# Optimization experiments

Hardware: AMD Instinct MI355X
Metric: run time of the kernel (lower is better)

## Reference

```python
import jax, jax.numpy as jnp
import numpy as np

EPS = 1e-3

def _block_orthogonal(num_rows, num_cols, seed=0):
    # Faithful to orthogonal_matrix(): stack of QR-orthogonalized square blocks.
    rng = np.random.default_rng(seed)
    blocks = []
    n_full = num_rows // num_cols
    for _ in range(n_full):
        q, _ = np.linalg.qr(rng.standard_normal((num_cols, num_cols)).astype(np.float32))
        blocks.append(q.T)
    remain = num_rows - n_full * num_cols
    if remain > 0:
        q, _ = np.linalg.qr(rng.standard_normal((num_cols, num_cols)).astype(np.float32))
        blocks.append(q.T[:remain])
    return jnp.asarray(np.concatenate(blocks, axis=0), dtype=jnp.float32)


def setup_inputs() -> dict:
    key = jax.random.key(0)
    k1, k2, k3 = jax.random.split(key, 3)
    B, H, L, D = 4, 16, 4096, 64
    num_rows = int(D * np.log(D))  # 266
    return {
        "q": jax.random.normal(k1, (B, H, L, D), dtype=jnp.float32),
        "k": jax.random.normal(k2, (B, H, L, D), dtype=jnp.float32),
        "v": jax.random.normal(k3, (B, H, L, D), dtype=jnp.float32),
        "proj_mat": _block_orthogonal(num_rows, D),  # [266, 64]
    }


def _feature_map(x, proj_t):
    # x: [b,h,l,d], proj_t: [d,m] -> [b,h,l,m]; kernel = relu, +epsilon
    return jax.nn.relu(jnp.einsum('bhld,dm->bhlm', x, proj_t)) + EPS


def reference(q, k, v, proj_mat):
    proj_t = proj_mat.T                     # [d, m]
    qp = _feature_map(q, proj_t)            # [b,h,l,m]
    kp = _feature_map(k, proj_t)            # [b,h,l,m]
    k_sum = jnp.sum(kp, axis=-2)            # [b,h,m]
    d_inv = 1.0 / jnp.einsum('bhlm,bhm->bhl', qp, k_sum)   # [b,h,l]
    kv = jnp.einsum('bhlm,bhld->bhmd', kp, v)              # [b,h,m,d]
    qkv = jnp.einsum('bhlm,bhmd->bhld', qp, kv)            # [b,h,l,d]
    return qkv * d_inv[..., None]
```

## Files before the change

### kernel.cpp

```cpp
#include <hip/hip_runtime.h>

typedef __bf16 bf16;
typedef bf16 bf16x2 __attribute__((ext_vector_type(2)));
typedef bf16 bf16x4 __attribute__((ext_vector_type(4)));
typedef bf16 bf16x8 __attribute__((ext_vector_type(8)));
typedef float f32x4 __attribute__((ext_vector_type(4)));
typedef float f32x16 __attribute__((ext_vector_type(16)));
typedef unsigned int u32;
typedef u32 u32x4 __attribute__((ext_vector_type(4)));
typedef float4 f4;

constexpr int BHN = 64;
constexpr int LN  = 4096;
constexpr int DN  = 64;
constexpr int MN  = 266;
constexpr int MP  = 320;
constexpr int STR = 72;
constexpr int KVS = 328;
constexpr int TL  = 128;
constexpr int NLQ = 4;
constexpr int NTQ = LN / (NLQ * TL);
#define EPSF 1e-3f

#define MFMA32(A, B, C) __builtin_amdgcn_mfma_f32_32x32x16_bf16(A, B, C, 0, 0, 0)

__device__ __forceinline__ u32 cvt_pk_bf16(float lo, float hi) {
  u32 r;
  asm("v_cvt_pk_bf16_f32 %0, %1, %2" : "=v"(r) : "v"(lo), "v"(hi));
  return r;
}

#define T12_TRANSFORM(f, kb0, kb1)                                   \
  {                                                                  \
    u32 w0 = cvt_pk_bf16(f[0], f[1]);                                \
    u32 w1 = cvt_pk_bf16(f[2], f[3]);                                \
    u32 w2 = cvt_pk_bf16(f[4], f[5]);                                \
    u32 w3 = cvt_pk_bf16(f[6], f[7]);                                \
    u32 w4 = cvt_pk_bf16(f[8], f[9]);                                \
    u32 w5 = cvt_pk_bf16(f[10], f[11]);                              \
    u32 w6 = cvt_pk_bf16(f[12], f[13]);                              \
    u32 w7 = cvt_pk_bf16(f[14], f[15]);                              \
    asm("v_permlane32_swap_b32 %0, %1" : "+v"(w0), "+v"(w2));        \
    asm("v_permlane32_swap_b32 %0, %1" : "+v"(w1), "+v"(w3));        \
    asm("v_permlane32_swap_b32 %0, %1" : "+v"(w4), "+v"(w6));        \
    asm("v_permlane32_swap_b32 %0, %1" : "+v"(w5), "+v"(w7));        \
    u32x4 a0_ = {w0, w1, w2, w3};                                    \
    u32x4 a1_ = {w4, w5, w6, w7};                                    \
    kb0 = __builtin_bit_cast(bf16x8, a0_);                           \
    kb1 = __builtin_bit_cast(bf16x8, a1_);                           \
  }

__global__ __launch_bounds__(640, 2) void perf_kv_fused(
    const float* __restrict__ kg, const float* __restrict__ vg,
    const float* __restrict__ proj, float* __restrict__ kv_part,
    float* __restrict__ ksum_part)
{
  __shared__ __align__(16) bf16 k_lds[TL * STR];
  __shared__ __align__(16) bf16 vt_lds[64 * 128];

  const int t    = threadIdx.x;
  const int wid  = t >> 6;
  const int lane = t & 63;
  const int ln31 = lane & 31;
  const int hi   = lane >> 5;
  const int mc   = wid % 5;
  const int h    = wid / 5;
  const int lq   = blockIdx.x & 3;
  const int bh   = blockIdx.x >> 2;
  const int m0   = mc * 64;

  bf16x8 pb[4];
  {
    const int m = m0 + h * 32 + ln31;
#pragma unroll
    for (int ks = 0; ks < 4; ++ks) {
      bf16x8 w = {};
      if (m < MN) {
        const float* p = proj + m * 64 + ks * 16 + hi * 8;
        f4 a = *(const f4*)p;
        f4 b = *(const f4*)(p + 4);
        w = (bf16x8){(bf16)a.x, (bf16)a.y, (bf16)a.z, (bf16)a.w,
                     (bf16)b.x, (bf16)b.y, (bf16)b.z, (bf16)b.w};
      }
      pb[ks] = w;
    }
  }

  f32x16 acc0 = (f32x16){};
  f32x16 acc1 = (f32x16){};
  float ksum_acc = 0.f;

  const f4* kg4 = (const f4*)kg + ((size_t)bh * LN) * 16;
  const f4* vg4 = (const f4*)vg + ((size_t)bh * LN) * 16;

  f4 kreg[4], vra[2], vrb[2];

  auto LOAD = [&](int tile) {
    const int l0 = (lq * NTQ + tile) * TL;
    if (t < 512) {
#pragma unroll
      for (int i2 = 0; i2 < 4; ++i2) {
        int idx = t + i2 * 512;
        kreg[i2] = kg4[(l0 + (idx >> 4)) * 16 + (idx & 15)];
      }
#pragma unroll
      for (int i2 = 0; i2 < 2; ++i2) {
        int u = t + i2 * 512;
        int lb2 = u >> 4, d4 = u & 15;
        vra[i2] = vg4[(l0 + lb2 * 2) * 16 + d4];
        vrb[i2] = vg4[(l0 + lb2 * 2 + 1) * 16 + d4];
      }
    }
  };
  auto VTW = [&](int r, int c) -> bf16* {
    return &vt_lds[r * 128 + (c ^ ((r & 15) << 3))];
  };
  auto WRITE = [&]() {
    if (t < 512) {
#pragma unroll
      for (int i2 = 0; i2 < 4; ++i2) {
        int idx = t + i2 * 512;
        int row = idx >> 4, d4 = idx & 15;
        f4 val = kreg[i2];
        bf16x4 w = {(bf16)val.x, (bf16)val.y, (bf16)val.z, (bf16)val.w};
        *(bf16x4*)&k_lds[row * STR + d4 * 4] = w;
      }
#pragma unroll
      for (int i2 = 0; i2 < 2; ++i2) {
        int u = t + i2 * 512;
        int lb2 = u >> 4, d4 = u & 15;
        f4 a = vra[i2], b = vrb[i2];
        bf16x2 w0 = {(bf16)a.x, (bf16)b.x};
        bf16x2 w1 = {(bf16)a.y, (bf16)b.y};
        bf16x2 w2 = {(bf16)a.z, (bf16)b.z};
        bf16x2 w3 = {(bf16)a.w, (bf16)b.w};
        *(bf16x2*)VTW(d4 * 4 + 0, lb2 * 2) = w0;
        *(bf16x2*)VTW(d4 * 4 + 1, lb2 * 2) = w1;
        *(bf16x2*)VTW(d4 * 4 + 2, lb2 * 2) = w2;
        *(bf16x2*)VTW(d4 * 4 + 3, lb2 * 2) = w3;
      }
    }
  };

  LOAD(0);
  for (int tile = 0; tile < NTQ; ++tile) {
    __syncthreads();
    WRITE();
    if (tile < NTQ - 1) LOAD(tile + 1);
    __syncthreads();

#pragma unroll
    for (int s4 = 0; s4 < 4; ++s4) {
      bf16x8 ka[4];
#pragma unroll
      for (int ks = 0; ks < 4; ++ks)
        ka[ks] = *(const bf16x8*)&k_lds[(s4 * 32 + ln31) * STR + ks * 16 + hi * 8];
      bf16x8 va00 = *(const bf16x8*)VTW(ln31, s4 * 32 + hi * 8);
      bf16x8 va01 = *(const bf16x8*)VTW(ln31, s4 * 32 + 16 + hi * 8);
      bf16x8 va10 = *(const bf16x8*)VTW(32 + ln31, s4 * 32 + hi * 8);
      bf16x8 va11 = *(const bf16x8*)VTW(32 + ln31, s4 * 32 + 16 + hi * 8);

      f32x16 f = (f32x16){};
#pragma unroll
      for (int ks = 0; ks < 4; ++ks) f = MFMA32(ka[ks], pb[ks], f);
#pragma unroll
      for (int i2 = 0; i2 < 16; ++i2) f[i2] = fmaxf(f[i2], 0.f) + EPSF;
      ksum_acc += f[0] + f[1] + f[2] + f[3] + f[4] + f[5] + f[6] + f[7]
                + f[8] + f[9] + f[10] + f[11] + f[12] + f[13] + f[14] + f[15];

      bf16x8 kb0, kb1;
      T12_TRANSFORM(f, kb0, kb1)
      acc0 = MFMA32(va00, kb0, acc0);
      acc0 = MFMA32(va01, kb1, acc0);
      acc1 = MFMA32(va10, kb0, acc1);
      acc1 = MFMA32(va11, kb1, acc1);
    }
  }

  {
    const int m = m0 + h * 32 + ln31;
    float* base = kv_part + ((size_t)lq * BHN + bh) * 64 * MP;
#pragma unroll
    for (int r = 0; r < 16; ++r) {
      const int d0 = (r & 3) + 8 * (r >> 2) + 4 * hi;
      base[(size_t)d0 * MP + m] = acc0[r];
      base[(size_t)(32 + d0) * MP + m] = acc1[r];
    }
    float rr = ksum_acc + __shfl_xor(ksum_acc, 32);
    if (hi == 0) ksum_part[((size_t)lq * BHN + bh) * MP + m] = rr;
  }
}

__global__ __launch_bounds__(256) void perf_reduce(
    const float* __restrict__ kv_part, const float* __restrict__ ksum_part,
    bf16* __restrict__ kv_b, float* __restrict__ ksum_ws)
{
  constexpr int KV4 = BHN * DN * MP / 4;
  constexpr int KS  = BHN * MP;
  constexpr size_t PS  = (size_t)BHN * DN * MP;
  constexpr size_t PSK = (size_t)BHN * MP;

  int idx = blockIdx.x * 256 + threadIdx.x;
  if (idx < KV4) {
    const f4* p = (const f4*)kv_part;
    f4 v0 = p[idx];
    f4 v1 = p[idx + PS / 4];
    f4 v2 = p[idx + 2 * (PS / 4)];
    f4 v3 = p[idx + 3 * (PS / 4)];
    f4 sv = {v0.x + v1.x + v2.x + v3.x, v0.y + v1.y + v2.y + v3.y,
             v0.z + v1.z + v2.z + v3.z, v0.w + v1.w + v2.w + v3.w};
    int m = (idx * 4) % MP;
    bf16x4 w;
    w[0] = (m + 0 < MN) ? (bf16)sv.x : (bf16)0.f;
    w[1] = (m + 1 < MN) ? (bf16)sv.y : (bf16)0.f;
    w[2] = (m + 2 < MN) ? (bf16)sv.z : (bf16)0.f;
    w[3] = (m + 3 < MN) ? (bf16)sv.w : (bf16)0.f;
    *(bf16x4*)&kv_b[idx * 4] = w;
  } else if (idx < KV4 + KS) {
    int p = idx - KV4;
    int m = p % MP;
    float v = ksum_part[p] + ksum_part[p + PSK] + ksum_part[p + 2 * PSK]
            + ksum_part[p + 3 * PSK];
    ksum_ws[p] = (m < MN) ? v : 0.f;
  }
}

__global__ __launch_bounds__(512, 2) void perf_out_mfma32(
    const float* __restrict__ qg, const float* __restrict__ proj,
    const bf16* __restrict__ kvb, const float* __restrict__ ksum_ws,
    float* __restrict__ outg)
{
  __shared__ __align__(16) bf16 pj_lds[MP * STR];
  __shared__ __align__(16) bf16 kv_lds[DN * KVS];
  __shared__ __align__(16) float ksum_lds[MP];
  __shared__ float dp_lds[8 * 64];

  const int t    = threadIdx.x;
  const int wid  = t >> 6;
  const int lane = t & 63;
  const int ln31 = lane & 31;
  const int hi   = lane >> 5;
  const int bh   = blockIdx.y;
  const int lbase = blockIdx.x * 1024;

  {
    const f4* projv = (const f4*)proj;
#pragma unroll
    for (int i = 0; i < 10; ++i) {
      int idx = t + i * 512;
      int r = idx >> 4, c4 = idx & 15;
      f4 v = {0.f, 0.f, 0.f, 0.f};
      if (r < MN) v = projv[r * 16 + c4];
      bf16x4 w = {(bf16)v.x, (bf16)v.y, (bf16)v.z, (bf16)v.w};
      *(bf16x4*)&pj_lds[r * STR + c4 * 4] = w;
    }
  }
  for (int idx = t; idx < DN * 40; idx += 512) {
    int r = idx / 40, cc = idx % 40;
    *(bf16x8*)&kv_lds[r * KVS + cc * 8] =
        *(const bf16x8*)&kvb[((size_t)bh * DN + r) * MP + cc * 8];
  }
  if (t < MP) ksum_lds[t] = ksum_ws[bh * MP + t];
  __syncthreads();

  for (int rnd = 0; rnd < 2; ++rnd) {
    const int lw = lbase + rnd * 512 + wid * 64;

    bf16x8 qb[2][4];
#pragma unroll
    for (int lt = 0; lt < 2; ++lt)
#pragma unroll
      for (int ks = 0; ks < 4; ++ks) {
        const float* qp_ = qg + ((size_t)bh * LN + lw + lt * 32 + ln31) * 64 + ks * 16 + hi * 8;
        f4 a = *(const f4*)qp_;
        f4 b = *(const f4*)(qp_ + 4);
        qb[lt][ks] = (bf16x8){(bf16)a.x, (bf16)a.y, (bf16)a.z, (bf16)a.w,
                              (bf16)b.x, (bf16)b.y, (bf16)b.z, (bf16)b.w};
      }

    f32x16 oc[2][2];
    oc[0][0] = (f32x16){}; oc[0][1] = (f32x16){};
    oc[1][0] = (f32x16){}; oc[1][1] = (f32x16){};
    float dp[2] = {0.f, 0.f};

    for (int mc = 0; mc < 5; ++mc) {
      f32x16 c2[2][2];
      c2[0][0] = (f32x16){}; c2[0][1] = (f32x16){};
      c2[1][0] = (f32x16){}; c2[1][1] = (f32x16){};
#pragma unroll
      for (int ks = 0; ks < 4; ++ks) {
        bf16x8 pa0 = *(const bf16x8*)&pj_lds[(mc * 64 + ln31) * STR + ks * 16 + hi * 8];
        bf16x8 pa1 = *(const bf16x8*)&pj_lds[(mc * 64 + 32 + ln31) * STR + ks * 16 + hi * 8];
        c2[0][0] = MFMA32(pa0, qb[0][ks], c2[0][0]);
        c2[1][0] = MFMA32(pa0, qb[1][ks], c2[1][0]);
        c2[0][1] = MFMA32(pa1, qb[0][ks], c2[0][1]);
        c2[1][1] = MFMA32(pa1, qb[1][ks], c2[1][1]);
      }
#pragma unroll
      for (int mt = 0; mt < 2; ++mt) {
        const int mb = mc * 64 + mt * 32 + 4 * hi;
        f32x4 kq0 = *(const f32x4*)&ksum_lds[mb + 0];
        f32x4 kq1 = *(const f32x4*)&ksum_lds[mb + 8];
        f32x4 kq2 = *(const f32x4*)&ksum_lds[mb + 16];
        f32x4 kq3 = *(const f32x4*)&ksum_lds[mb + 24];
        bf16x8 A[2][2];
#pragma unroll
        for (int lt = 0; lt < 2; ++lt) {
          f32x16 f = c2[lt][mt];
#pragma unroll
          for (int i = 0; i < 16; ++i) f[i] = fmaxf(f[i], 0.f) + EPSF;
          dp[lt] += f[0] * kq0[0] + f[1] * kq0[1] + f[2] * kq0[2] + f[3] * kq0[3]
                  + f[4] * kq1[0] + f[5] * kq1[1] + f[6] * kq1[2] + f[7] * kq1[3]
                  + f[8] * kq2[0] + f[9] * kq2[1] + f[10] * kq2[2] + f[11] * kq2[3]
                  + f[12] * kq3[0] + f[13] * kq3[1] + f[14] * kq3[2] + f[15] * kq3[3];
          bf16x8 kb0, kb1;
          T12_TRANSFORM(f, kb0, kb1)
          A[lt][0] = kb0;
          A[lt][1] = kb1;
        }
#pragma unroll
        for (int kk = 0; kk < 2; ++kk) {
          const int mo = mc * 64 + (mt * 2 + kk) * 16 + hi * 8;
          bf16x8 kb0 = *(const bf16x8*)&kv_lds[ln31 * KVS + mo];
          bf16x8 kb1 = *(const bf16x8*)&kv_lds[(32 + ln31) * KVS + mo];
          oc[0][0] = MFMA32(A[0][kk], kb0, oc[0][0]);
          oc[1][0] = MFMA32(A[1][kk], kb0, oc[1][0]);
          oc[0][1] = MFMA32(A[0][kk], kb1, oc[0][1]);
          oc[1][1] = MFMA32(A[1][kk], kb1, oc[1][1]);
        }
      }
    }

#pragma unroll
    for (int lt = 0; lt < 2; ++lt) {
      float r = dp[lt];
      r += __shfl_xor(r, 32);
      dp_lds[wid * 64 + lt * 32 + ln31] = r;
    }
#pragma unroll
    for (int lt = 0; lt < 2; ++lt) {
#pragma unroll
      for (int rg = 0; rg < 4; ++rg) {
        f32x4 dv = *(const f32x4*)&dp_lds[wid * 64 + lt * 32 + 8 * rg + 4 * hi];
        f32x4 di = {1.f / dv[0], 1.f / dv[1], 1.f / dv[2], 1.f / dv[3]};
#pragma unroll
        for (int dt = 0; dt < 2; ++dt) {
#pragma unroll
          for (int j = 0; j < 4; ++j) {
            int l = lw + lt * 32 + 8 * rg + 4 * hi + j;
            outg[((size_t)bh * LN + l) * DN + dt * 32 + ln31] = oc[lt][dt][4 * rg + j] * di[j];
          }
        }
      }
    }
  }
}

extern "C" void kernel_launch(void* const* d_in, const int* in_sizes, int n_in,
                              void* d_out, int out_size, void* d_ws, size_t ws_size,
                              hipStream_t stream)
{
  const float* q    = (const float*)d_in[0];
  const float* k    = (const float*)d_in[1];
  const float* v    = (const float*)d_in[2];
  const float* proj = (const float*)d_in[3];
  float* out = (float*)d_out;

  float* kv_part   = (float*)d_ws;
  float* ksum_part = kv_part + (size_t)NLQ * BHN * DN * MP;
  float* ksum_ws   = ksum_part + (size_t)NLQ * BHN * MP;
  bf16*  kv_b      = (bf16*)(ksum_ws + (size_t)BHN * MP);

  perf_kv_fused<<<NLQ * BHN, 640, 0, stream>>>(k, v, proj, kv_part, ksum_part);

  constexpr int RED_ITEMS = BHN * DN * MP / 4 + BHN * MP;
  perf_reduce<<<(RED_ITEMS + 255) / 256, 256, 0, stream>>>(kv_part, ksum_part, kv_b, ksum_ws);

  perf_out_mfma32<<<dim3(LN / 1024, BHN), 512, 0, stream>>>(q, proj, kv_b, ksum_ws, out);
}
```

Baseline: 91.58 us.

## Double-buffer K/V LDS tiles to drop one barrier per tile

```diff
diff --git a/kernel.cpp b/kernel.cpp
--- a/kernel.cpp
+++ b/kernel.cpp
@@ -55,8 +55,8 @@
     const float* __restrict__ proj, float* __restrict__ kv_part,
     float* __restrict__ ksum_part)
 {
-  __shared__ __align__(16) bf16 k_lds[TL * STR];
-  __shared__ __align__(16) bf16 vt_lds[64 * 128];
+  __shared__ __align__(16) bf16 k_lds[2][TL * STR];
+  __shared__ __align__(16) bf16 vt_lds[2][64 * 128];
 
   const int t    = threadIdx.x;
   const int wid  = t >> 6;
@@ -112,10 +112,10 @@
       }
     }
   };
-  auto VTW = [&](int r, int c) -> bf16* {
-    return &vt_lds[r * 128 + (c ^ ((r & 15) << 3))];
+  auto VTW = [&](int b, int r, int c) -> bf16* {
+    return &vt_lds[b][r * 128 + (c ^ ((r & 15) << 3))];
   };
-  auto WRITE = [&]() {
+  auto WRITE = [&](int b) {
     if (t < 512) {
 #pragma unroll
       for (int i2 = 0; i2 < 4; ++i2) {
@@ -123,42 +123,48 @@
         int row = idx >> 4, d4 = idx & 15;
         f4 val = kreg[i2];
         bf16x4 w = {(bf16)val.x, (bf16)val.y, (bf16)val.z, (bf16)val.w};
-        *(bf16x4*)&k_lds[row * STR + d4 * 4] = w;
+        *(bf16x4*)&k_lds[b][row * STR + d4 * 4] = w;
       }
 #pragma unroll
       for (int i2 = 0; i2 < 2; ++i2) {
         int u = t + i2 * 512;
         int lb2 = u >> 4, d4 = u & 15;
-        f4 a = vra[i2], b = vrb[i2];
-        bf16x2 w0 = {(bf16)a.x, (bf16)b.x};
-        bf16x2 w1 = {(bf16)a.y, (bf16)b.y};
-        bf16x2 w2 = {(bf16)a.z, (bf16)b.z};
-        bf16x2 w3 = {(bf16)a.w, (bf16)b.w};
-        *(bf16x2*)VTW(d4 * 4 + 0, lb2 * 2) = w0;
-        *(bf16x2*)VTW(d4 * 4 + 1, lb2 * 2) = w1;
-        *(bf16x2*)VTW(d4 * 4 + 2, lb2 * 2) = w2;
-        *(bf16x2*)VTW(d4 * 4 + 3, lb2 * 2) = w3;
+        f4 a = vra[i2], b2 = vrb[i2];
+        bf16x2 w0 = {(bf16)a.x, (bf16)b2.x};
+        bf16x2 w1 = {(bf16)a.y, (bf16)b2.y};
+        bf16x2 w2 = {(bf16)a.z, (bf16)b2.z};
+        bf16x2 w3 = {(bf16)a.w, (bf16)b2.w};
+        *(bf16x2*)VTW(b, d4 * 4 + 0, lb2 * 2) = w0;
+        *(bf16x2*)VTW(b, d4 * 4 + 1, lb2 * 2) = w1;
+        *(bf16x2*)VTW(b, d4 * 4 + 2, lb2 * 2) = w2;
+        *(bf16x2*)VTW(b, d4 * 4 + 3, lb2 * 2) = w3;
       }
     }
   };
 
   LOAD(0);
+  WRITE(0);
+  LOAD(1);
+
   for (int tile = 0; tile < NTQ; ++tile) {
+    const int cur = tile & 1;
     __syncthreads();
-    WRITE();
-    if (tile < NTQ - 1) LOAD(tile + 1);
-    __syncthreads();
+
+    if (tile + 1 < NTQ) {
+      WRITE(cur ^ 1);
+      if (tile + 2 < NTQ) LOAD(tile + 2);
+    }
 
 #pragma unroll
     for (int s4 = 0; s4 < 4; ++s4) {
       bf16x8 ka[4];
 #pragma unroll
       for (int ks = 0; ks < 4; ++ks)
-        ka[ks] = *(const bf16x8*)&k_lds[(s4 * 32 + ln31) * STR + ks * 16 + hi * 8];
-      bf16x8 va00 = *(const bf16x8*)VTW(ln31, s4 * 32 + hi * 8);
-      bf16x8 va01 = *(const bf16x8*)VTW(ln31, s4 * 32 + 16 + hi * 8);
-      bf16x8 va10 = *(const bf16x8*)VTW(32 + ln31, s4 * 32 + hi * 8);
-      bf16x8 va11 = *(const bf16x8*)VTW(32 + ln31, s4 * 32 + 16 + hi * 8);
+        ka[ks] = *(const bf16x8*)&k_lds[cur][(s4 * 32 + ln31) * STR + ks * 16 + hi * 8];
+      bf16x8 va00 = *(const bf16x8*)VTW(cur, ln31, s4 * 32 + hi * 8);
+      bf16x8 va01 = *(const bf16x8*)VTW(cur, ln31, s4 * 32 + 16 + hi * 8);
+      bf16x8 va10 = *(const bf16x8*)VTW(cur, 32 + ln31, s4 * 32 + hi * 8);
+      bf16x8 va11 = *(const bf16x8*)VTW(cur, 32 + ln31, s4 * 32 + 16 + hi * 8);
 
       f32x16 f = (f32x16){};
 #pragma unroll
```

After: 102.0 us. +11.3%, slower.
